# Kernel optimization log

Hardware: AMD Instinct MI355X
Metric: run time of the kernel (lower is better)

The kernel has to match this reference:

```python
import jax, jax.numpy as jnp
import numpy as np

N_NODES = 100000
N_EDGES = 1000000
F_IN = 64
F_HID = 64
F_OUT = 2
NUM_GRAPHS = 64


def setup_inputs() -> dict:
    key = jax.random.key(0)
    ks = jax.random.split(key, 8)
    x = jax.random.normal(ks[0], (N_NODES, F_IN), dtype=jnp.float32)
    edge_index = jax.random.randint(ks[1], (2, N_EDGES), 0, N_NODES, dtype=jnp.int32)
    batch = jnp.sort(jax.random.randint(ks[2], (N_NODES,), 0, NUM_GRAPHS, dtype=jnp.int32))
    s1 = 1.0 / np.sqrt(F_IN)
    s2 = 1.0 / np.sqrt(F_HID)
    W1 = jax.random.normal(ks[3], (F_IN, F_HID), dtype=jnp.float32) * s1
    W2 = jax.random.normal(ks[4], (F_HID, F_HID), dtype=jnp.float32) * s2
    W3 = jax.random.normal(ks[5], (F_HID, F_HID), dtype=jnp.float32) * s2
    Wlin = jax.random.normal(ks[6], (F_HID, F_OUT), dtype=jnp.float32) * s2
    return {
        "x": x, "edge_index": edge_index, "batch": batch,
        "W1": W1, "b1": jnp.zeros((F_HID,), jnp.float32),
        "W2": W2, "b2": jnp.zeros((F_HID,), jnp.float32),
        "W3": W3, "b3": jnp.zeros((F_HID,), jnp.float32),
        "Wlin": Wlin, "blin": jnp.zeros((F_OUT,), jnp.float32),
    }


def _gcn_norm(edge_index, n_nodes):
    # add self-loops, compute symmetric D^-1/2 (A+I) D^-1/2 edge weights
    loops = jnp.arange(n_nodes, dtype=edge_index.dtype)
    src = jnp.concatenate([edge_index[0], loops])  # message source j
    dst = jnp.concatenate([edge_index[1], loops])  # aggregation target i
    deg = jax.ops.segment_sum(jnp.ones_like(dst, dtype=jnp.float32), dst,
                              num_segments=n_nodes)
    dinv = jnp.where(deg > 0, jax.lax.rsqrt(deg), 0.0)
    norm = dinv[src] * dinv[dst]  # [E+N]
    return src, dst, norm


def _gcn_conv(h, W, b, src, dst, norm, n_nodes):
    h = h @ W                                    # [N, F] dense transform first (PyG order)
    msg = h[src] * norm[:, None]                 # gather + scale  [E+N, F]
    agg = jax.ops.segment_sum(msg, dst, num_segments=n_nodes)
    return agg + b


def reference(x, edge_index, batch, W1, b1, W2, b2, W3, b3, Wlin, blin):
    n = x.shape[0]
    src, dst, norm = _gcn_norm(edge_index, n)
    h = jax.nn.relu(_gcn_conv(x, W1, b1, src, dst, norm, n))
    h = jax.nn.relu(_gcn_conv(h, W2, b2, src, dst, norm, n))
    h = _gcn_conv(h, W3, b3, src, dst, norm, n)
    # global mean pool over graphs
    sums = jax.ops.segment_sum(h, batch, num_segments=NUM_GRAPHS)        # [G, F]
    cnts = jax.ops.segment_sum(jnp.ones((n,), jnp.float32), batch,
                               num_segments=NUM_GRAPHS)
    pooled = sums / jnp.maximum(cnts, 1.0)[:, None]
    # dropout(p=0.1) is identity in eval mode
    return pooled @ Wlin + blin
```

## Files before the change

kernel.cpp:

```cpp
#include <hip/hip_runtime.h>

#define FDIM 64

typedef unsigned short u16;
typedef unsigned int u32;
typedef float v2f __attribute__((ext_vector_type(2)));

__device__ __forceinline__ u32 pk_fp8x4(float a, float b, float c, float d) {
    u32 p = __builtin_amdgcn_cvt_pk_fp8_f32(a, b, 0, false);
    p = __builtin_amdgcn_cvt_pk_fp8_f32(c, d, p, true);
    return p;
}


template <bool SCALE>
__device__ __forceinline__ void mm_compute(
    u32* __restrict__ t, const int* __restrict__ cnt, int n, int r0,
    float (*__restrict__ As)[FDIM + 1], const float* __restrict__ Ws)
{
    int tid = threadIdx.x;
    int rq = tid >> 4;
    int cq = tid & 15;
    float acc[4][4];
    #pragma unroll
    for (int i = 0; i < 4; ++i)
        #pragma unroll
        for (int j = 0; j < 4; ++j) acc[i][j] = 0.f;

    const float4* Ws4 = (const float4*)Ws;
    #pragma unroll 4
    for (int k = 0; k < FDIM; ++k) {
        float4 w = Ws4[k * 16 + cq];
        float a[4];
        #pragma unroll
        for (int i = 0; i < 4; ++i) a[i] = As[rq * 4 + i][k];
        #pragma unroll
        for (int i = 0; i < 4; ++i) {
            acc[i][0] = fmaf(a[i], w.x, acc[i][0]);
            acc[i][1] = fmaf(a[i], w.y, acc[i][1]);
            acc[i][2] = fmaf(a[i], w.z, acc[i][2]);
            acc[i][3] = fmaf(a[i], w.w, acc[i][3]);
        }
    }

    #pragma unroll
    for (int i = 0; i < 4; ++i) {
        int R = r0 + rq * 4 + i;
        if (R < n) {
            float sc = 1.0f;
            if (SCALE) sc = rsqrtf((float)cnt[R] + 1.0f);
            t[(size_t)R * 16 + cq] =
                pk_fp8x4(acc[i][0] * sc, acc[i][1] * sc,
                         acc[i][2] * sc, acc[i][3] * sc);
        }
    }
}


__global__ __launch_bounds__(256) void k_mm_fill(
    const float* __restrict__ x, const float* __restrict__ W1,
    u32* __restrict__ t,
    const int* __restrict__ src, const int* __restrict__ dst,
    int* __restrict__ cnt, int* __restrict__ csr,
    int n, int E, int cap, int fill_blocks)
{
    __shared__ float As[64][FDIM + 1];
    __shared__ float Ws[FDIM * FDIM];

    if ((int)blockIdx.x < fill_blocks) {
        int stride = fill_blocks * 256;
        int e = blockIdx.x * 256 + threadIdx.x;
        for (; e + 7 * stride < E; e += 8 * stride) {
            int d[8], s[8], p[8];
            #pragma unroll
            for (int u = 0; u < 8; ++u)
                d[u] = __builtin_nontemporal_load(&dst[e + u * stride]);
            #pragma unroll
            for (int u = 0; u < 8; ++u)
                s[u] = __builtin_nontemporal_load(&src[e + u * stride]);
            #pragma unroll
            for (int u = 0; u < 8; ++u) p[u] = atomicAdd(&cnt[d[u]], 1);
            #pragma unroll
            for (int u = 0; u < 8; ++u)
                if (p[u] < cap) csr[(size_t)d[u] * cap + p[u]] = s[u];
        }
        for (; e < E; e += stride) {
            int d = dst[e];
            int p = atomicAdd(&cnt[d], 1);
            if (p < cap) csr[(size_t)d * cap + p] = src[e];
        }
        return;
    }

    int blk = blockIdx.x - fill_blocks;
    int r0 = blk * 64;
    int tid = threadIdx.x;
    #pragma unroll
    for (int i = 0; i < 4; ++i)
        ((float4*)Ws)[tid + 256 * i] = ((const float4*)W1)[tid + 256 * i];

    #pragma unroll
    for (int i = 0; i < 4; ++i) {
        int idx = tid + 256 * i;
        int r = idx >> 4;
        int kq = idx & 15;
        float4 v = make_float4(0.f, 0.f, 0.f, 0.f);
        int R = r0 + r;
        if (R < n) v = ((const float4*)x)[(size_t)R * 16 + kq];
        As[r][kq * 4 + 0] = v.x;
        As[r][kq * 4 + 1] = v.y;
        As[r][kq * 4 + 2] = v.z;
        As[r][kq * 4 + 3] = v.w;
    }
    __syncthreads();
    mm_compute<false>(t, nullptr, n, r0, As, Ws);
}


template <bool SCALED>
__device__ __forceinline__ float4 agg_node(
    int i, const int* __restrict__ cnt, const int* __restrict__ csr,
    const u32* __restrict__ t, int cap, int li, int nbase)
{
    int dg = cnt[i];
    float di = rsqrtf((float)dg + 1.0f);
    int m = dg < cap ? dg : cap;

    u32 sp = t[(size_t)i * 16 + li];
    v2f s0 = __builtin_amdgcn_cvt_pk_f32_fp8(sp, false);
    v2f s1 = __builtin_amdgcn_cvt_pk_f32_fp8(sp, true);
    float4 A0, A1, A2, A3;
    if (SCALED) {
        A0 = make_float4(s0.x, s0.y, s1.x, s1.y);
    } else {
        A0 = make_float4(s0.x * di, s0.y * di, s1.x * di, s1.y * di);
    }
    A1 = make_float4(0.f, 0.f, 0.f, 0.f);
    A2 = make_float4(0.f, 0.f, 0.f, 0.f);
    A3 = make_float4(0.f, 0.f, 0.f, 0.f);

    const int* row = csr + (size_t)i * cap;

    for (int c0 = 0; c0 < m; c0 += 16) {
        int cm = m - c0; if (cm > 16) cm = 16;
        int sv = -1; float dvv = 0.f;
        if (li < cm) {
            sv = __builtin_nontemporal_load(&row[c0 + li]);
            if (!SCALED) dvv = rsqrtf((float)cnt[sv] + 1.0f);
        }
        int jv[16]; float dj[16]; u32 v[16];
        #pragma unroll
        for (int u = 0; u < 16; ++u) {
            jv[u] = __shfl(sv, nbase + u);
            if (!SCALED) dj[u] = __shfl(dvv, nbase + u);
        }
        #pragma unroll
        for (int u = 0; u < 16; ++u)
            v[u] = t[(long long)jv[u] * 16 + li];
        #pragma unroll
        for (int u = 0; u < 16; ++u) {
            v2f x0 = __builtin_amdgcn_cvt_pk_f32_fp8(v[u], false);
            v2f x1 = __builtin_amdgcn_cvt_pk_f32_fp8(v[u], true);
            float4* Ap = (u & 3) == 0 ? &A0 : (u & 3) == 1 ? &A1 :
                         (u & 3) == 2 ? &A2 : &A3;
            if (SCALED) {
                Ap->x += x0.x; Ap->y += x0.y;
                Ap->z += x1.x; Ap->w += x1.y;
            } else {
                Ap->x = fmaf(x0.x, dj[u], Ap->x);
                Ap->y = fmaf(x0.y, dj[u], Ap->y);
                Ap->z = fmaf(x1.x, dj[u], Ap->z);
                Ap->w = fmaf(x1.y, dj[u], Ap->w);
            }
        }
    }

    float4 O;
    O.x = ((A0.x + A1.x) + (A2.x + A3.x)) * di;
    O.y = ((A0.y + A1.y) + (A2.y + A3.y)) * di;
    O.z = ((A0.z + A1.z) + (A2.z + A3.z)) * di;
    O.w = ((A0.w + A1.w) + (A2.w + A3.w)) * di;
    return O;
}


template <bool SCALED_IN>
__global__ __launch_bounds__(256) void k_aggmm(
    const int* __restrict__ cnt, const int* __restrict__ csr,
    const u32* __restrict__ tin, const float* __restrict__ Wm,
    const float* __restrict__ bias, u32* __restrict__ tout,
    int n, int cap)
{
    __shared__ float As[64][FDIM + 1];
    __shared__ float Ws[FDIM * FDIM];
    int tid = threadIdx.x;
    #pragma unroll
    for (int i = 0; i < 4; ++i)
        ((float4*)Ws)[tid + 256 * i] = ((const float4*)Wm)[tid + 256 * i];

    int r0 = blockIdx.x * 64;
    int group = tid >> 4;
    int li = tid & 15;
    int nbase = ((tid & 63) >> 4) << 4;
    float4 b = ((const float4*)bias)[li];

    #pragma unroll 1
    for (int r = 0; r < 4; ++r) {
        int row = r * 16 + group;
        int i = r0 + row;
        float4 v = make_float4(0.f, 0.f, 0.f, 0.f);
        if (i < n) {
            float4 O = agg_node<SCALED_IN>(i, cnt, csr, tin, cap, li, nbase);
            v.x = fmaxf(O.x + b.x, 0.f);
            v.y = fmaxf(O.y + b.y, 0.f);
            v.z = fmaxf(O.z + b.z, 0.f);
            v.w = fmaxf(O.w + b.w, 0.f);
        }
        As[row][li * 4 + 0] = v.x;
        As[row][li * 4 + 1] = v.y;
        As[row][li * 4 + 2] = v.z;
        As[row][li * 4 + 3] = v.w;
    }
    __syncthreads();
    mm_compute<true>(tout, cnt, n, r0, As, Ws);
}


__global__ __launch_bounds__(256) void k_agg_pool(
    const int* __restrict__ cnt, const int* __restrict__ csr,
    const u32* __restrict__ t, const int* __restrict__ batch,
    float* __restrict__ partial, int n, int cap, int npart)
{
    int g = blockIdx.x / npart;
    int part = blockIdx.x - g * npart;
    int tid = threadIdx.x;

    int lo = 0, hi = n;
    while (lo < hi) { int mid = (lo + hi) >> 1; if (batch[mid] < g) lo = mid + 1; else hi = mid; }
    int start = lo;
    hi = n;
    while (lo < hi) { int mid = (lo + hi) >> 1; if (batch[mid] <= g) lo = mid + 1; else hi = mid; }
    int end = lo;

    int group = tid >> 4;
    int li = tid & 15;
    int nbase = ((tid & 63) >> 4) << 4;

    float4 acc = make_float4(0.f, 0.f, 0.f, 0.f);
    for (int i = start + part * 16 + group; i < end; i += npart * 16) {
        float4 O = agg_node<true>(i, cnt, csr, t, cap, li, nbase);
        acc.x += O.x; acc.y += O.y; acc.z += O.z; acc.w += O.w;
    }

    __shared__ float4 red[16][16];
    red[group][li] = acc;
    __syncthreads();
    if (tid < 16) {
        float4 s = make_float4(0.f, 0.f, 0.f, 0.f);
        #pragma unroll
        for (int q = 0; q < 16; ++q) {
            s.x += red[q][tid].x; s.y += red[q][tid].y;
            s.z += red[q][tid].z; s.w += red[q][tid].w;
        }
        ((float4*)partial)[((size_t)g * npart + part) * 16 + tid] = s;
    }
}


__global__ __launch_bounds__(64) void k_pool2(
    const float* __restrict__ partial, const int* __restrict__ batch,
    const float* __restrict__ b3, const float* __restrict__ Wlin,
    const float* __restrict__ blin, float* __restrict__ out,
    int n, int fout, int npart)
{
    int g = blockIdx.x;
    int tid = threadIdx.x;

    int lo = 0, hi = n;
    while (lo < hi) { int mid = (lo + hi) >> 1; if (batch[mid] < g) lo = mid + 1; else hi = mid; }
    int start = lo;
    hi = n;
    while (lo < hi) { int mid = (lo + hi) >> 1; if (batch[mid] <= g) lo = mid + 1; else hi = mid; }
    int cg = lo - start;

    __shared__ float pooled[64];
    float v = 0.f;
    for (int p = 0; p < npart; ++p)
        v += partial[((size_t)g * npart + p) * 64 + tid];
    pooled[tid] = (cg > 0) ? (v / (float)cg + b3[tid]) : 0.f;
    __syncthreads();
    if (tid < fout) {
        float o = blin[tid];
        for (int k = 0; k < 64; ++k) o += pooled[k] * Wlin[k * fout + tid];
        out[(size_t)g * fout + tid] = o;
    }
}


extern "C" void kernel_launch(void* const* d_in, const int* in_sizes, int n_in,
                              void* d_out, int out_size, void* d_ws, size_t ws_size,
                              hipStream_t stream) {
    const float* x     = (const float*)d_in[0];
    const int*   ei    = (const int*)d_in[1];
    const int*   batch = (const int*)d_in[2];
    const float* W1 = (const float*)d_in[3];
    const float* b1 = (const float*)d_in[4];
    const float* W2 = (const float*)d_in[5];
    const float* b2 = (const float*)d_in[6];
    const float* W3 = (const float*)d_in[7];
    const float* b3 = (const float*)d_in[8];
    const float* Wl = (const float*)d_in[9];
    const float* bl = (const float*)d_in[10];

    int n = in_sizes[0] / 64;
    int E = in_sizes[1] / 2;
    int fout = in_sizes[10];
    int ngraphs = out_size / fout;

    const int* srcp = ei;
    const int* dstp = ei + E;

    const int npart = 16;

    int* cnt = (int*)d_ws;
    u32* zA  = (u32*)(cnt + n);
    u32* tA  = zA + 16;
    u32* zB  = tA + (size_t)n * 16;
    u32* tB  = zB + 16;
    float* partial = (float*)(tB + (size_t)n * 16);
    int* csr = (int*)(partial + (size_t)ngraphs * npart * 64);

    size_t fixed = (size_t)n * 4 + 128 + (size_t)n * 128 +
                   (size_t)ngraphs * npart * 64 * 4;
    int cap = 64;
    while (cap > 32 && fixed + (size_t)n * cap * 4 > ws_size) cap -= 8;

    int mm_blocks = (n + 63) / 64;
    int fill_blocks = 256;

    size_t mset = (size_t)n * 4 + 64 + (size_t)n * 64 + 64;
    hipMemsetAsync(cnt, 0, mset, stream);
    k_mm_fill<<<fill_blocks + mm_blocks, 256, 0, stream>>>(
        x, W1, tA, srcp, dstp, cnt, csr, n, E, cap, fill_blocks);

    k_aggmm<false><<<mm_blocks, 256, 0, stream>>>(cnt, csr, tA, W2, b1, tB, n, cap);
    k_aggmm<true><<<mm_blocks, 256, 0, stream>>>(cnt, csr, tB, W3, b2, tA, n, cap);
    k_agg_pool<<<ngraphs * npart, 256, 0, stream>>>(
        cnt, csr, tA, batch, partial, n, cap, npart);
    k_pool2<<<ngraphs, 64, 0, stream>>>(partial, batch, b3, Wl, bl,
                                        (float*)d_out, n, fout, npart);
}
```

Before: 253.0 us.

## Software-pipeline neighbor gathers across nodes in aggregation kernels

Rewrites the aggregation in k_aggmm and k_agg_pool so that the first 16-neighbor gather for the next node is issued before the current node's accumulation is consumed. Two register buffers alternate, which hides gather latency across nodes. The pooling kernel doubles npart to add more blocks, and the memset is narrowed to the count array and zero-pad sentinels instead of clearing the tA feature buffer. This raises register pressure and could lower occupancy.

```diff
diff --git a/kernel.cpp b/kernel.cpp
--- a/kernel.cpp
+++ b/kernel.cpp
@@ -117,71 +117,12 @@
 }
 
 
-template <bool SCALED>
-__device__ __forceinline__ float4 agg_node(
-    int i, const int* __restrict__ cnt, const int* __restrict__ csr,
-    const u32* __restrict__ t, int cap, int li, int nbase)
-{
-    int dg = cnt[i];
-    float di = rsqrtf((float)dg + 1.0f);
-    int m = dg < cap ? dg : cap;
-
-    u32 sp = t[(size_t)i * 16 + li];
-    v2f s0 = __builtin_amdgcn_cvt_pk_f32_fp8(sp, false);
-    v2f s1 = __builtin_amdgcn_cvt_pk_f32_fp8(sp, true);
-    float4 A0, A1, A2, A3;
-    if (SCALED) {
-        A0 = make_float4(s0.x, s0.y, s1.x, s1.y);
-    } else {
-        A0 = make_float4(s0.x * di, s0.y * di, s1.x * di, s1.y * di);
-    }
-    A1 = make_float4(0.f, 0.f, 0.f, 0.f);
-    A2 = make_float4(0.f, 0.f, 0.f, 0.f);
-    A3 = make_float4(0.f, 0.f, 0.f, 0.f);
-
-    const int* row = csr + (size_t)i * cap;
-
-    for (int c0 = 0; c0 < m; c0 += 16) {
-        int cm = m - c0; if (cm > 16) cm = 16;
-        int sv = -1; float dvv = 0.f;
-        if (li < cm) {
-            sv = __builtin_nontemporal_load(&row[c0 + li]);
-            if (!SCALED) dvv = rsqrtf((float)cnt[sv] + 1.0f);
-        }
-        int jv[16]; float dj[16]; u32 v[16];
-        #pragma unroll
-        for (int u = 0; u < 16; ++u) {
-            jv[u] = __shfl(sv, nbase + u);
-            if (!SCALED) dj[u] = __shfl(dvv, nbase + u);
-        }
-        #pragma unroll
-        for (int u = 0; u < 16; ++u)
-            v[u] = t[(long long)jv[u] * 16 + li];
-        #pragma unroll
-        for (int u = 0; u < 16; ++u) {
-            v2f x0 = __builtin_amdgcn_cvt_pk_f32_fp8(v[u], false);
-            v2f x1 = __builtin_amdgcn_cvt_pk_f32_fp8(v[u], true);
-            float4* Ap = (u & 3) == 0 ? &A0 : (u & 3) == 1 ? &A1 :
-                         (u & 3) == 2 ? &A2 : &A3;
-            if (SCALED) {
-                Ap->x += x0.x; Ap->y += x0.y;
-                Ap->z += x1.x; Ap->w += x1.y;
-            } else {
-                Ap->x = fmaf(x0.x, dj[u], Ap->x);
-                Ap->y = fmaf(x0.y, dj[u], Ap->y);
-                Ap->z = fmaf(x1.x, dj[u], Ap->z);
-                Ap->w = fmaf(x1.y, dj[u], Ap->w);
-            }
-        }
-    }
-
-    float4 O;
-    O.x = ((A0.x + A1.x) + (A2.x + A3.x)) * di;
-    O.y = ((A0.y + A1.y) + (A2.y + A3.y)) * di;
-    O.z = ((A0.z + A1.z) + (A2.z + A3.z)) * di;
-    O.w = ((A0.w + A1.w) + (A2.w + A3.w)) * di;
-    return O;
-}
+#define GATH(T, SVV, BUF) do {                                             \
+    _Pragma("unroll")                                                      \
+    for (int u_ = 0; u_ < 16; ++u_) {                                      \
+        int jv_ = __shfl((SVV), nbase + u_);                               \
+        BUF[u_] = (T)[(long long)jv_ * 16 + li];                           \
+    } } while (0)
 
 
 template <bool SCALED_IN>
@@ -204,23 +145,101 @@
     int nbase = ((tid & 63) >> 4) << 4;
     float4 b = ((const float4*)bias)[li];
 
-    #pragma unroll 1
+    int mN[4]; float diN[4]; int svN[4]; int cvN[4]; u32 spN[4];
+    #pragma unroll
     for (int r = 0; r < 4; ++r) {
-        int row = r * 16 + group;
-        int i = r0 + row;
-        float4 v = make_float4(0.f, 0.f, 0.f, 0.f);
-        if (i < n) {
-            float4 O = agg_node<SCALED_IN>(i, cnt, csr, tin, cap, li, nbase);
-            v.x = fmaxf(O.x + b.x, 0.f);
-            v.y = fmaxf(O.y + b.y, 0.f);
-            v.z = fmaxf(O.z + b.z, 0.f);
-            v.w = fmaxf(O.w + b.w, 0.f);
-        }
-        As[row][li * 4 + 0] = v.x;
-        As[row][li * 4 + 1] = v.y;
-        As[row][li * 4 + 2] = v.z;
-        As[row][li * 4 + 3] = v.w;
-    }
+        int i = r0 + r * 16 + group;
+        bool ok = i < n;
+        int ic = ok ? i : 0;
+        int dg = cnt[ic];
+        diN[r] = rsqrtf((float)dg + 1.0f);
+        int m = ok ? (dg < cap ? dg : cap) : 0;
+        mN[r] = m;
+        spN[r] = tin[(long long)(ok ? i : -1) * 16 + li];
+        int cm = m < 16 ? m : 16;
+        int sv = -1;
+        if (li < cm) sv = __builtin_nontemporal_load(&csr[(size_t)ic * cap + li]);
+        svN[r] = sv;
+        cvN[r] = 0;
+        if (!SCALED_IN && li < cm) cvN[r] = cnt[sv];
+    }
+
+    u32 vb0[16], vb1[16];
+
+#define CONSUME_MM(R, BUF) do {                                            \
+    int m_ = mN[R]; float di_ = diN[R];                                    \
+    v2f s0_ = __builtin_amdgcn_cvt_pk_f32_fp8(spN[R], false);              \
+    v2f s1_ = __builtin_amdgcn_cvt_pk_f32_fp8(spN[R], true);               \
+    float4 A0, A1, A2, A3;                                                 \
+    if (SCALED_IN) A0 = make_float4(s0_.x, s0_.y, s1_.x, s1_.y);           \
+    else A0 = make_float4(s0_.x * di_, s0_.y * di_, s1_.x * di_, s1_.y * di_); \
+    A1 = make_float4(0.f, 0.f, 0.f, 0.f); A2 = A1; A3 = A1;                \
+    float dvv_ = SCALED_IN ? 0.f : rsqrtf((float)cvN[R] + 1.0f);           \
+    _Pragma("unroll")                                                      \
+    for (int u = 0; u < 16; ++u) {                                         \
+        v2f x0 = __builtin_amdgcn_cvt_pk_f32_fp8(BUF[u], false);           \
+        v2f x1 = __builtin_amdgcn_cvt_pk_f32_fp8(BUF[u], true);            \
+        float4* Ap = (u & 3) == 0 ? &A0 : (u & 3) == 1 ? &A1 :             \
+                     (u & 3) == 2 ? &A2 : &A3;                             \
+        if (SCALED_IN) {                                                   \
+            Ap->x += x0.x; Ap->y += x0.y; Ap->z += x1.x; Ap->w += x1.y;    \
+        } else {                                                           \
+            float dj_ = __shfl(dvv_, nbase + u);                           \
+            Ap->x = fmaf(x0.x, dj_, Ap->x); Ap->y = fmaf(x0.y, dj_, Ap->y);\
+            Ap->z = fmaf(x1.x, dj_, Ap->z); Ap->w = fmaf(x1.y, dj_, Ap->w);\
+        }                                                                  \
+    }                                                                      \
+    if (m_ > 16) {                \
+        const int* row_ = csr + (size_t)(r0 + (R) * 16 + group) * cap;     \
+        for (int c0 = 16; c0 < m_; c0 += 16) {                             \
+            int cm2 = m_ - c0; if (cm2 > 16) cm2 = 16;                     \
+            int sv2 = -1; float dv2 = 0.f;                                 \
+            if (li < cm2) {                                                \
+                sv2 = __builtin_nontemporal_load(&row_[c0 + li]);          \
+                if (!SCALED_IN) dv2 = rsqrtf((float)cnt[sv2] + 1.0f);      \
+            }                                                              \
+            GATH(tin, sv2, BUF);                                           \
+            _Pragma("unroll")                                              \
+            for (int u = 0; u < 16; ++u) {                                 \
+                v2f x0 = __builtin_amdgcn_cvt_pk_f32_fp8(BUF[u], false);   \
+                v2f x1 = __builtin_amdgcn_cvt_pk_f32_fp8(BUF[u], true);    \
+                float4* Ap = (u & 3) == 0 ? &A0 : (u & 3) == 1 ? &A1 :     \
+                             (u & 3) == 2 ? &A2 : &A3;                     \
+                if (SCALED_IN) {                                           \
+                    Ap->x += x0.x; Ap->y += x0.y;                          \
+                    Ap->z += x1.x; Ap->w += x1.y;                          \
+                } else {                                                   \
+                    float dj2 = __shfl(dv2, nbase + u);                    \
+                    Ap->x = fmaf(x0.x, dj2, Ap->x);                        \
+                    Ap->y = fmaf(x0.y, dj2, Ap->y);                        \
+                    Ap->z = fmaf(x1.x, dj2, Ap->z);                        \
+                    Ap->w = fmaf(x1.y, dj2, Ap->w);                        \
+                }                                                          \
+            }                                                              \
+        }                                                                  \
+    }                                                                      \
+    float4 O_;                                                             \
+    O_.x = ((A0.x + A1.x) + (A2.x + A3.x)) * di_;                          \
+    O_.y = ((A0.y + A1.y) + (A2.y + A3.y)) * di_;                          \
+    O_.z = ((A0.z + A1.z) + (A2.z + A3.z)) * di_;                          \
+    O_.w = ((A0.w + A1.w) + (A2.w + A3.w)) * di_;                          \
+    int row2_ = (R) * 16 + group;                                          \
+    As[row2_][li * 4 + 0] = fmaxf(O_.x + b.x, 0.f);                        \
+    As[row2_][li * 4 + 1] = fmaxf(O_.y + b.y, 0.f);                        \
+    As[row2_][li * 4 + 2] = fmaxf(O_.z + b.z, 0.f);                        \
+    As[row2_][li * 4 + 3] = fmaxf(O_.w + b.w, 0.f);                        \
+} while (0)
+
+    GATH(tin, svN[0], vb0);
+    GATH(tin, svN[1], vb1);
+    CONSUME_MM(0, vb0);
+    GATH(tin, svN[2], vb0);
+    CONSUME_MM(1, vb1);
+    GATH(tin, svN[3], vb1);
+    CONSUME_MM(2, vb0);
+    CONSUME_MM(3, vb1);
+#undef CONSUME_MM
+
     __syncthreads();
     mm_compute<true>(tout, cnt, n, r0, As, Ws);
 }
@@ -246,11 +265,85 @@
     int li = tid & 15;
     int nbase = ((tid & 63) >> 4) << 4;
 
+#define LCTX(II, M, DI, SV, SP) do {                                       \
+    (M) = 0; (DI) = 0.f; (SV) = -1; (SP) = 0u;                             \
+    if ((II) < end) {                                                      \
+        int dg_ = cnt[(II)];                                               \
+        (DI) = rsqrtf((float)dg_ + 1.0f);                                  \
+        (M) = dg_ < cap ? dg_ : cap;                                       \
+        (SP) = t[(size_t)(II) * 16 + li];                                  \
+        int cm_ = (M) < 16 ? (M) : 16;                                     \
+        if (li < cm_) (SV) = __builtin_nontemporal_load(                   \
+                                 &csr[(size_t)(II) * cap + li]);           \
+    } } while (0)
+
+#define CONSUME_P(M_, DI_, SP_, II_, BUF) do {                             \
+    v2f s0_ = __builtin_amdgcn_cvt_pk_f32_fp8((SP_), false);               \
+    v2f s1_ = __builtin_amdgcn_cvt_pk_f32_fp8((SP_), true);                \
+    float4 A0 = make_float4(s0_.x, s0_.y, s1_.x, s1_.y);                   \
+    float4 A1 = make_float4(0.f, 0.f, 0.f, 0.f), A2 = A1, A3 = A1;         \
+    _Pragma("unroll")                                                      \
+    for (int u = 0; u < 16; ++u) {                                         \
+        v2f x0 = __builtin_amdgcn_cvt_pk_f32_fp8(BUF[u], false);           \
+        v2f x1 = __builtin_amdgcn_cvt_pk_f32_fp8(BUF[u], true);            \
+        float4* Ap = (u & 3) == 0 ? &A0 : (u & 3) == 1 ? &A1 :             \
+                     (u & 3) == 2 ? &A2 : &A3;                             \
+        Ap->x += x0.x; Ap->y += x0.y; Ap->z += x1.x; Ap->w += x1.y;        \
+    }                                                                      \
+    if ((M_) > 16) {                                                       \
+        const int* row_ = csr + (size_t)(II_) * cap;                       \
+        for (int c0 = 16; c0 < (M_); c0 += 16) {                           \
+            int cm2 = (M_) - c0; if (cm2 > 16) cm2 = 16;                   \
+            int sv2 = -1;                                                  \
+            if (li < cm2) sv2 = __builtin_nontemporal_load(&row_[c0 + li]);\
+            GATH(t, sv2, BUF);                                             \
+            _Pragma("unroll")                                              \
+            for (int u = 0; u < 16; ++u) {                                 \
+                v2f x0 = __builtin_amdgcn_cvt_pk_f32_fp8(BUF[u], false);   \
+                v2f x1 = __builtin_amdgcn_cvt_pk_f32_fp8(BUF[u], true);    \
+                float4* Ap = (u & 3) == 0 ? &A0 : (u & 3) == 1 ? &A1 :     \
+                             (u & 3) == 2 ? &A2 : &A3;                     \
+                Ap->x += x0.x; Ap->y += x0.y; Ap->z += x1.x; Ap->w += x1.y;\
+            }                                                              \
+        }                                                                  \
+    }                                                                      \
+    acc.x += ((A0.x + A1.x) + (A2.x + A3.x)) * (DI_);                      \
+    acc.y += ((A0.y + A1.y) + (A2.y + A3.y)) * (DI_);                      \
+    acc.z += ((A0.z + A1.z) + (A2.z + A3.z)) * (DI_);                      \
+    acc.w += ((A0.w + A1.w) + (A2.w + A3.w)) * (DI_);                      \
+} while (0)
+
+    const int S = npart * 16;
     float4 acc = make_float4(0.f, 0.f, 0.f, 0.f);
-    for (int i = start + part * 16 + group; i < end; i += npart * 16) {
-        float4 O = agg_node<true>(i, cnt, csr, t, cap, li, nbase);
-        acc.x += O.x; acc.y += O.y; acc.z += O.z; acc.w += O.w;
-    }
+    int i = start + part * 16 + group;
+
+    int mA, svA, iiA; float diA; u32 spA;
+    int mB, svB, iiB; float diB; u32 spB;
+    int mT, svT, iiT; float diT; u32 spT;
+    u32 vb0[16], vb1[16];
+
+    iiA = i;     LCTX(iiA, mA, diA, svA, spA);
+    iiB = i + S; LCTX(iiB, mB, diB, svB, spB);
+    GATH(t, svA, vb0);
+
+    while (i < end) {
+        GATH(t, svB, vb1);
+        iiT = i + 2 * S; LCTX(iiT, mT, diT, svT, spT);
+        CONSUME_P(mA, diA, spA, iiA, vb0);
+        mA = mB; diA = diB; svA = svB; spA = spB; iiA = iiB;
+        mB = mT; diB = diT; svB = svT; spB = spT; iiB = iiT;
+        i += S;
+        if (i >= end) break;
+
+        GATH(t, svB, vb0);
+        iiT = i + 2 * S; LCTX(iiT, mT, diT, svT, spT);
+        CONSUME_P(mA, diA, spA, iiA, vb1);
+        mA = mB; diA = diB; svA = svB; spA = spB; iiA = iiB;
+        mB = mT; diB = diT; svB = svT; spB = spT; iiB = iiT;
+        i += S;
+    }
+#undef CONSUME_P
+#undef LCTX
 
     __shared__ float4 red[16][16];
     red[group][li] = acc;
@@ -320,7 +413,7 @@
     const int* srcp = ei;
     const int* dstp = ei + E;
 
-    const int npart = 16;
+    const int npart = 32;
 
     int* cnt = (int*)d_ws;
     u32* zA  = (u32*)(cnt + n);
@@ -338,8 +431,8 @@
     int mm_blocks = (n + 63) / 64;
     int fill_blocks = 256;
 
-    size_t mset = (size_t)n * 4 + 64 + (size_t)n * 64 + 64;
-    hipMemsetAsync(cnt, 0, mset, stream);
+    hipMemsetAsync(cnt, 0, (size_t)n * 4 + 64, stream);
+    hipMemsetAsync(zB, 0, 64, stream);
     k_mm_fill<<<fill_blocks + mm_blocks, 256, 0, stream>>>(
         x, W1, tA, srcp, dstp, cnt, csr, n, E, cap, fill_blocks);
 
```

New measurement: 270.7 us. 7.0% more time.

## Build compact CSR via bucketed counting sort instead of padded atomic fill

Applied to the files above, without the earlier changes.

Replaces the global-atomic padded adjacency fill (fixed cap per node) with a two-level counting sort: per-block bucket histograms over dst>>8, a prefix scan, a scatter of packed (dst,src) pairs into buckets, then per-bucket local sorting into a compact CSR with row pointers. Aggregation kernels now read rows through rptr with exact degree, so there is no cap truncation and the CSR is denser. The aim is to cut random global atomics and scattered writes. In exchange it adds three extra launches, a single-block serial scan, and an extra pass over 8-byte edge pairs.

```diff
diff --git a/kernel.cpp b/kernel.cpp
--- a/kernel.cpp
+++ b/kernel.cpp
@@ -4,6 +4,7 @@
 
 typedef unsigned short u16;
 typedef unsigned int u32;
+typedef unsigned long long u64;
 typedef float v2f __attribute__((ext_vector_type(2)));
 
 __device__ __forceinline__ u32 pk_fp8x4(float a, float b, float c, float d) {
@@ -57,48 +58,115 @@
 }
 
 
-__global__ __launch_bounds__(256) void k_mm_fill(
+__global__ __launch_bounds__(256) void k_hist(
+    const int* __restrict__ dst, int* __restrict__ hpart, int E, int nbuk)
+{
+    __shared__ int h[1024];
+    int tid = threadIdx.x, blk = blockIdx.x;
+    for (int b = tid; b < nbuk; b += 256) h[b] = 0;
+    __syncthreads();
+    int stride = gridDim.x * 256;
+    for (int e = blk * 256 + tid; e < E; e += stride)
+        atomicAdd(&h[dst[e] >> 8], 1);
+    __syncthreads();
+    for (int b = tid; b < nbuk; b += 256) hpart[b * 256 + blk] = h[b];
+}
+
+__global__ __launch_bounds__(256) void k_scan(
+    int* __restrict__ hpart, int* __restrict__ bb, int nbuk)
+{
+    __shared__ int tot[1024];
+    int tid = threadIdx.x;
+    for (int b = tid; b < nbuk; b += 256) {
+        int* col = hpart + (size_t)b * 256;
+        int r = 0;
+        for (int k = 0; k < 256; ++k) { int v = col[k]; col[k] = r; r += v; }
+        tot[b] = r;
+    }
+    __syncthreads();
+    if (tid == 0) {
+        int r = 0;
+        for (int b = 0; b < nbuk; ++b) { int v = tot[b]; tot[b] = r; r += v; }
+        bb[nbuk] = r;
+    }
+    __syncthreads();
+    for (int b = tid; b < nbuk; b += 256) {
+        int base = tot[b];
+        bb[b] = base;
+        int* col = hpart + (size_t)b * 256;
+        for (int k = 0; k < 256; ++k) col[k] += base;
+    }
+}
+
+__global__ __launch_bounds__(256) void k_scatter(
+    const int* __restrict__ src, const int* __restrict__ dst,
+    const int* __restrict__ hpart, u64* __restrict__ ebuf, int E, int nbuk)
+{
+    __shared__ int cur[1024];
+    int tid = threadIdx.x, blk = blockIdx.x;
+    for (int b = tid; b < nbuk; b += 256) cur[b] = hpart[(size_t)b * 256 + blk];
+    __syncthreads();
+    int stride = gridDim.x * 256;
+    for (int e = blk * 256 + tid; e < E; e += stride) {
+        int d = dst[e], s = src[e];
+        int p = atomicAdd(&cur[d >> 8], 1);
+        ebuf[p] = ((u64)(u32)d << 32) | (u32)s;
+    }
+}
+
+__global__ __launch_bounds__(256) void k_build_mm(
+    const u64* __restrict__ ebuf, const int* __restrict__ bb,
+    int* __restrict__ cnt, int* __restrict__ rptr, int* __restrict__ csr,
     const float* __restrict__ x, const float* __restrict__ W1,
-    u32* __restrict__ t,
-    const int* __restrict__ src, const int* __restrict__ dst,
-    int* __restrict__ cnt, int* __restrict__ csr,
-    int n, int E, int cap, int fill_blocks)
+    u32* __restrict__ t, int n, int nbuk)
 {
     __shared__ float As[64][FDIM + 1];
     __shared__ float Ws[FDIM * FDIM];
-
-    if ((int)blockIdx.x < fill_blocks) {
-        int stride = fill_blocks * 256;
-        int e = blockIdx.x * 256 + threadIdx.x;
-        for (; e + 7 * stride < E; e += 8 * stride) {
-            int d[8], s[8], p[8];
-            #pragma unroll
-            for (int u = 0; u < 8; ++u)
-                d[u] = __builtin_nontemporal_load(&dst[e + u * stride]);
-            #pragma unroll
-            for (int u = 0; u < 8; ++u)
-                s[u] = __builtin_nontemporal_load(&src[e + u * stride]);
-            #pragma unroll
-            for (int u = 0; u < 8; ++u) p[u] = atomicAdd(&cnt[d[u]], 1);
-            #pragma unroll
-            for (int u = 0; u < 8; ++u)
-                if (p[u] < cap) csr[(size_t)d[u] * cap + p[u]] = s[u];
-        }
-        for (; e < E; e += stride) {
-            int d = dst[e];
-            int p = atomicAdd(&cnt[d], 1);
-            if (p < cap) csr[(size_t)d * cap + p] = src[e];
+    __shared__ int cnt_l[256], scn[256], cur[256];
+
+    int tid = threadIdx.x;
+    if ((int)blockIdx.x < nbuk) {
+        int b = blockIdx.x;
+        int node0 = b << 8;
+        int nn = n - node0; if (nn > 256) nn = 256;
+        int e0 = bb[b], e1 = bb[b + 1];
+
+        cnt_l[tid] = 0;
+        __syncthreads();
+        for (int e = e0 + tid; e < e1; e += 256)
+            atomicAdd(&cnt_l[(int)(ebuf[e] >> 32) & 255], 1);
+        __syncthreads();
+        int v = cnt_l[tid];
+        scn[tid] = v;
+        __syncthreads();
+        #pragma unroll
+        for (int off = 1; off < 256; off <<= 1) {
+            int w = (tid >= off) ? scn[tid - off] : 0;
+            __syncthreads();
+            scn[tid] += w;
+            __syncthreads();
+        }
+        int excl = scn[tid] - v;
+        if (tid < nn) {
+            cnt[node0 + tid]  = v;
+            rptr[node0 + tid] = e0 + excl;
+        }
+        cur[tid] = e0 + excl;
+        __syncthreads();
+        for (int e = e0 + tid; e < e1; e += 256) {
+            u64 pk = ebuf[e];
+            int local = (int)(pk >> 32) & 255;
+            int p = atomicAdd(&cur[local], 1);
+            csr[p] = (int)(u32)(pk & 0xffffffffu);
         }
         return;
     }
 
-    int blk = blockIdx.x - fill_blocks;
+    int blk = blockIdx.x - nbuk;
     int r0 = blk * 64;
-    int tid = threadIdx.x;
     #pragma unroll
     for (int i = 0; i < 4; ++i)
         ((float4*)Ws)[tid + 256 * i] = ((const float4*)W1)[tid + 256 * i];
-
     #pragma unroll
     for (int i = 0; i < 4; ++i) {
         int idx = tid + 256 * i;
@@ -119,12 +187,13 @@
 
 template <bool SCALED>
 __device__ __forceinline__ float4 agg_node(
-    int i, const int* __restrict__ cnt, const int* __restrict__ csr,
-    const u32* __restrict__ t, int cap, int li, int nbase)
+    int i, const int* __restrict__ cnt, const int* __restrict__ rptr,
+    const int* __restrict__ csr, const u32* __restrict__ t,
+    int li, int nbase)
 {
     int dg = cnt[i];
     float di = rsqrtf((float)dg + 1.0f);
-    int m = dg < cap ? dg : cap;
+    int m = dg;
 
     u32 sp = t[(size_t)i * 16 + li];
     v2f s0 = __builtin_amdgcn_cvt_pk_f32_fp8(sp, false);
@@ -139,7 +208,7 @@
     A2 = make_float4(0.f, 0.f, 0.f, 0.f);
     A3 = make_float4(0.f, 0.f, 0.f, 0.f);
 
-    const int* row = csr + (size_t)i * cap;
+    const int* row = csr + rptr[i];
 
     for (int c0 = 0; c0 < m; c0 += 16) {
         int cm = m - c0; if (cm > 16) cm = 16;
@@ -186,10 +255,10 @@
 
 template <bool SCALED_IN>
 __global__ __launch_bounds__(256) void k_aggmm(
-    const int* __restrict__ cnt, const int* __restrict__ csr,
-    const u32* __restrict__ tin, const float* __restrict__ Wm,
-    const float* __restrict__ bias, u32* __restrict__ tout,
-    int n, int cap)
+    const int* __restrict__ cnt, const int* __restrict__ rptr,
+    const int* __restrict__ csr, const u32* __restrict__ tin,
+    const float* __restrict__ Wm, const float* __restrict__ bias,
+    u32* __restrict__ tout, int n)
 {
     __shared__ float As[64][FDIM + 1];
     __shared__ float Ws[FDIM * FDIM];
@@ -210,7 +279,7 @@
         int i = r0 + row;
         float4 v = make_float4(0.f, 0.f, 0.f, 0.f);
         if (i < n) {
-            float4 O = agg_node<SCALED_IN>(i, cnt, csr, tin, cap, li, nbase);
+            float4 O = agg_node<SCALED_IN>(i, cnt, rptr, csr, tin, li, nbase);
             v.x = fmaxf(O.x + b.x, 0.f);
             v.y = fmaxf(O.y + b.y, 0.f);
             v.z = fmaxf(O.z + b.z, 0.f);
@@ -227,9 +296,10 @@
 
 
 __global__ __launch_bounds__(256) void k_agg_pool(
-    const int* __restrict__ cnt, const int* __restrict__ csr,
-    const u32* __restrict__ t, const int* __restrict__ batch,
-    float* __restrict__ partial, int n, int cap, int npart)
+    const int* __restrict__ cnt, const int* __restrict__ rptr,
+    const int* __restrict__ csr, const u32* __restrict__ t,
+    const int* __restrict__ batch, float* __restrict__ partial,
+    int n, int npart)
 {
     int g = blockIdx.x / npart;
     int part = blockIdx.x - g * npart;
@@ -248,7 +318,7 @@
 
     float4 acc = make_float4(0.f, 0.f, 0.f, 0.f);
     for (int i = start + part * 16 + group; i < end; i += npart * 16) {
-        float4 O = agg_node<true>(i, cnt, csr, t, cap, li, nbase);
+        float4 O = agg_node<true>(i, cnt, rptr, csr, t, li, nbase);
         acc.x += O.x; acc.y += O.y; acc.z += O.z; acc.w += O.w;
     }
 
@@ -321,32 +391,35 @@
     const int* dstp = ei + E;
 
     const int npart = 16;
-
-    int* cnt = (int*)d_ws;
-    u32* zA  = (u32*)(cnt + n);
+    int nbuk = (n + 255) >> 8;
+
+    u64* ebuf = (u64*)d_ws;
+    int* csr  = (int*)(ebuf + (size_t)E);
+    int* cnt  = csr + (size_t)E;
+    int* rptr = cnt + n;
+    int* bb   = rptr + n;
+    int* hpart = bb + (nbuk + 1);
+    u32* zA  = (u32*)(hpart + (size_t)nbuk * 256);
     u32* tA  = zA + 16;
     u32* zB  = tA + (size_t)n * 16;
     u32* tB  = zB + 16;
-    float* partial = (float*)(tB + (size_t)n * 16);
-    int* csr = (int*)(partial + (size_t)ngraphs * npart * 64);
-
-    size_t fixed = (size_t)n * 4 + 128 + (size_t)n * 128 +
-                   (size_t)ngraphs * npart * 64 * 4;
-    int cap = 64;
-    while (cap > 32 && fixed + (size_t)n * cap * 4 > ws_size) cap -= 8;
+    float* ppool = (float*)(tB + (size_t)n * 16);
 
     int mm_blocks = (n + 63) / 64;
-    int fill_blocks = 256;
-
-    size_t mset = (size_t)n * 4 + 64 + (size_t)n * 64 + 64;
-    hipMemsetAsync(cnt, 0, mset, stream);
-    k_mm_fill<<<fill_blocks + mm_blocks, 256, 0, stream>>>(
-        x, W1, tA, srcp, dstp, cnt, csr, n, E, cap, fill_blocks);
-
-    k_aggmm<false><<<mm_blocks, 256, 0, stream>>>(cnt, csr, tA, W2, b1, tB, n, cap);
-    k_aggmm<true><<<mm_blocks, 256, 0, stream>>>(cnt, csr, tB, W3, b2, tA, n, cap);
+
+    hipMemsetAsync(zA, 0, 64, stream);
+    hipMemsetAsync(zB, 0, 64, stream);
+
+    k_hist<<<256, 256, 0, stream>>>(dstp, hpart, E, nbuk);
+    k_scan<<<1, 256, 0, stream>>>(hpart, bb, nbuk);
+    k_scatter<<<256, 256, 0, stream>>>(srcp, dstp, hpart, ebuf, E, nbuk);
+    k_build_mm<<<nbuk + mm_blocks, 256, 0, stream>>>(
+        ebuf, bb, cnt, rptr, csr, x, W1, tA, n, nbuk);
+
+    k_aggmm<false><<<mm_blocks, 256, 0, stream>>>(cnt, rptr, csr, tA, W2, b1, tB, n);
+    k_aggmm<true><<<mm_blocks, 256, 0, stream>>>(cnt, rptr, csr, tB, W3, b2, tA, n);
     k_agg_pool<<<ngraphs * npart, 256, 0, stream>>>(
-        cnt, csr, tA, batch, partial, n, cap, npart);
-    k_pool2<<<ngraphs, 64, 0, stream>>>(partial, batch, b3, Wl, bl,
+        cnt, rptr, csr, tA, batch, ppool, n, npart);
+    k_pool2<<<ngraphs, 64, 0, stream>>>(ppool, batch, b3, Wl, bl,
                                         (float*)d_out, n, fout, npart);
 }
```

Measured after the change: 306.2 us. 1.21x slower.
